# Optimization experiments

Hardware: AMD Instinct MI355X
Metric: run time of the kernel (lower is better)

The kernel has to match this reference:

```python
import jax, jax.numpy as jnp
import numpy as np

B, N, M, E, C_IN, C_OUT = 4, 10000, 10000, 160000, 128, 128


def setup_inputs() -> dict:
    key = jax.random.key(0)
    k1, k2, k3, k4 = jax.random.split(key, 4)
    x = jax.random.normal(k1, (B, N, C_IN), dtype=jnp.float32)
    node_idx = jax.random.randint(k2, (B, 1, E), 0, N)
    hyedge_idx = jax.random.randint(k3, (B, 1, E), 0, M)
    H = jnp.concatenate([node_idx, hyedge_idx], axis=1).astype(jnp.int64)  # [B, 2, E]
    theta = jax.random.normal(k4, (C_IN, C_OUT), dtype=jnp.float32) * (1.0 / np.sqrt(C_IN))
    bias = jnp.zeros((C_OUT,), dtype=jnp.float32)
    return {"x": x, "H": H, "theta": theta, "bias": bias}


def _hyconv_single(xg, Hg):
    # xg: [N, D] (already x @ theta); Hg: [2, E]
    node_idx, hyedge_idx = Hg[0], Hg[1]
    ones = jnp.ones((E,), dtype=xg.dtype)
    # node -> hyperedge: mean over nodes incident to each hyperedge
    deg_e = jax.ops.segment_sum(ones, hyedge_idx, num_segments=M)  # [M]
    e_norm = (1.0 / deg_e)[hyedge_idx]  # [E]
    x_edge = jax.ops.segment_sum(xg[node_idx] * e_norm[:, None], hyedge_idx, num_segments=M)  # [M, D]
    # hyperedge -> node: mean over hyperedges incident to each node
    deg_n = jax.ops.segment_sum(ones, node_idx, num_segments=N)  # [N]
    n_norm = (1.0 / deg_n)[node_idx]  # [E]
    x_node = jax.ops.segment_sum(x_edge[hyedge_idx] * n_norm[:, None], node_idx, num_segments=N)  # [N, D]
    return x_node


def reference(x, H, theta, bias):
    xt = jnp.einsum('bnc,cd->bnd', x, theta)  # dense projection
    out = jax.vmap(_hyconv_single)(xt, H)  # [B, N, D]
    return out + bias
```

## Files before the change

kernel.cpp:

```cpp
#include <hip/hip_runtime.h>
#include <hip/hip_bf16.h>


#define BB 4
#define NN 10000
#define MM 10000
#define EE 160000
#define CC 128
#define BM (BB * MM)
#define BN (BB * NN)
#define NCOPY 8
#define CAPX 16

typedef unsigned short u16;
using bf16 = __hip_bfloat16;
using bf162 = __hip_bfloat162;
typedef unsigned u32x4 __attribute__((ext_vector_type(4)));
typedef float f32x4 __attribute__((ext_vector_type(4)));

__global__ __launch_bounds__(256) void build_gemm_k(const int* __restrict__ H,
                                                    int* __restrict__ ctr,
                                                    u16* __restrict__ srcA,
                                                    u16* __restrict__ srcB,
                                                    const float* __restrict__ x,
                                                    const float* __restrict__ theta,
                                                    bf16* __restrict__ xt) {
    __shared__ float sTh[64 * 128];
    __shared__ float sX[32 * 128];
    const int bi = blockIdx.x;
    const int idx = (bi >> 4) * 8 + (bi & 7);

    if ((bi >> 3) & 1) {
        if (idx >= 1250) return;
        const int gidx = idx * 256 + threadIdx.x;
        const int g0 = gidx * 2;
        const int cp = bi & 7;
        const int b = g0 / EE, e = g0 - b * EE;
        const int2 nd2 = *(const int2*)&H[b * 2 * EE + e];
        const int2 he2 = *(const int2*)&H[b * 2 * EE + EE + e];
        {
            const int bktA = b * MM + he2.x;
            const int s = atomicAdd(&ctr[cp * (BM + BN) + bktA], 1);
            if (s < CAPX) srcA[((size_t)cp * BM + bktA) * CAPX + s] = (u16)nd2.x;
            const int bktB = b * NN + nd2.x;
            const int q = atomicAdd(&ctr[cp * (BM + BN) + BM + bktB], 1);
            if (q < CAPX) srcB[((size_t)cp * BN + bktB) * CAPX + q] = (u16)he2.x;
        }
        {
            const int bktA = b * MM + he2.y;
            const int s = atomicAdd(&ctr[cp * (BM + BN) + bktA], 1);
            if (s < CAPX) srcA[((size_t)cp * BM + bktA) * CAPX + s] = (u16)nd2.y;
            const int bktB = b * NN + nd2.y;
            const int q = atomicAdd(&ctr[cp * (BM + BN) + BM + bktB], 1);
            if (q < CAPX) srcB[((size_t)cp * BN + bktB) * CAPX + q] = (u16)he2.y;
        }
        return;
    }

    if (idx >= 1250) return;
    const int tid = threadIdx.x;
    const int row0 = idx * 32;
    {
        const float4* src = (const float4*)&x[row0 * 128];
        float4* dst = (float4*)sX;
#pragma unroll
        for (int i = 0; i < 4; ++i) dst[tid + 256 * i] = src[tid + 256 * i];
    }
    const int cg2 = (tid & 63) * 2;
    const int rg = tid >> 6;
    float ax[8], ay[8];
#pragma unroll
    for (int r = 0; r < 8; ++r) { ax[r] = 0.f; ay[r] = 0.f; }

    for (int half = 0; half < 2; ++half) {
        __syncthreads();
        {
            const float4* src = (const float4*)&theta[half * 64 * 128];
            float4* dst = (float4*)sTh;
#pragma unroll
            for (int i = 0; i < 8; ++i) dst[tid + 256 * i] = src[tid + 256 * i];
        }
        __syncthreads();
#pragma unroll
        for (int k4 = 0; k4 < 16; ++k4) {
            const int kk = 4 * k4;
            const float2 t0 = *(const float2*)&sTh[(kk + 0) * 128 + cg2];
            const float2 t1 = *(const float2*)&sTh[(kk + 1) * 128 + cg2];
            const float2 t2 = *(const float2*)&sTh[(kk + 2) * 128 + cg2];
            const float2 t3 = *(const float2*)&sTh[(kk + 3) * 128 + cg2];
#pragma unroll
            for (int r = 0; r < 8; ++r) {
                const float4 xv =
                    *(const float4*)&sX[(rg * 8 + r) * 128 + half * 64 + kk];
                ax[r] = fmaf(xv.x, t0.x, ax[r]); ay[r] = fmaf(xv.x, t0.y, ay[r]);
                ax[r] = fmaf(xv.y, t1.x, ax[r]); ay[r] = fmaf(xv.y, t1.y, ay[r]);
                ax[r] = fmaf(xv.z, t2.x, ax[r]); ay[r] = fmaf(xv.z, t2.y, ay[r]);
                ax[r] = fmaf(xv.w, t3.x, ax[r]); ay[r] = fmaf(xv.w, t3.y, ay[r]);
            }
        }
    }
#pragma unroll
    for (int r = 0; r < 8; ++r) {
        bf162 h;
        h.x = __float2bfloat16(ax[r]);
        h.y = __float2bfloat16(ay[r]);
        *(bf162*)&xt[(size_t)(row0 + rg * 8 + r) * 128 + cg2] = h;
    }
}

__device__ __forceinline__ float blo(unsigned w) { return __uint_as_float(w << 16); }
__device__ __forceinline__ float bhi(unsigned w) { return __uint_as_float(w & 0xffff0000u); }
__device__ __forceinline__ unsigned pk2(float a, float b) {
    bf162 h;
    h.x = __float2bfloat16(a);
    h.y = __float2bfloat16(b);
    return *(unsigned*)&h;
}

__device__ __forceinline__ void acc8(const uint4 pk, float* s) {
    s[0] += blo(pk.x); s[1] += bhi(pk.x);
    s[2] += blo(pk.y); s[3] += bhi(pk.y);
    s[4] += blo(pk.z); s[5] += bhi(pk.z);
    s[6] += blo(pk.w); s[7] += bhi(pk.w);
}

__device__ __forceinline__ void swz_bucket(int blk, int tid, int& b, int& wid_local4) {
    const int xcd = blk & 7;
    b = xcd >> 1;
    const int jj = ((blk >> 3) << 1) | (xcd & 1);
    wid_local4 = jj * 4 + (tid >> 6);
}

__global__ __launch_bounds__(256) void phase1_pull(const bf16* __restrict__ xt,
                                                   const int* __restrict__ ctr,
                                                   const u16* __restrict__ srcA,
                                                   const u16* __restrict__ srcB,
                                                   u16* __restrict__ flatB,
                                                   int* __restrict__ cntB,
                                                   bf16* __restrict__ x_edge) {
    __shared__ __align__(16) u16 bufA[4 * 64];
    __shared__ __align__(16) u16 bufB[4 * 64];
    int b, wl;
    swz_bucket(blockIdx.x, threadIdx.x, b, wl);
    const int widA = b * MM + wl;
    const int widB = b * NN + wl;
    const int lane = threadIdx.x & 63;
    const int w4 = threadIdx.x >> 6;
    u16* wbufA = &bufA[w4 * 64];
    u16* wbufB = &bufB[w4 * 64];

    int cA = 0, cB = 0;
    uint4 a0, a1, b0, b1;
    if (lane < NCOPY) {
        const u16* la = srcA + ((size_t)lane * BM + widA) * CAPX;
        const u16* lb = srcB + ((size_t)lane * BN + widB) * CAPX;
        a0 = *(const uint4*)la; a1 = *(const uint4*)(la + 8);
        b0 = *(const uint4*)lb; b1 = *(const uint4*)(lb + 8);
        cA = ctr[lane * (BM + BN) + widA];       cA = cA > CAPX ? CAPX : cA;
        cB = ctr[lane * (BM + BN) + BM + widB];  cB = cB > CAPX ? CAPX : cB;
    }
    int pA = cA, pB = cB;
#pragma unroll
    for (int d = 1; d < 8; d <<= 1) {
        const int oA = __shfl_up(pA, d, 64);
        const int oB = __shfl_up(pB, d, 64);
        if (lane >= d) { pA += oA; pB += oB; }
    }
    const int baseA = pA - cA, baseB = pB - cB;
    int totA = __shfl(pA, 7, 64); totA = totA > 64 ? 64 : totA;
    int totB = __shfl(pB, 7, 64); totB = totB > 64 ? 64 : totB;
    if (lane < NCOPY) {
        const unsigned wa[8] = {a0.x, a0.y, a0.z, a0.w, a1.x, a1.y, a1.z, a1.w};
        const unsigned wb[8] = {b0.x, b0.y, b0.z, b0.w, b1.x, b1.y, b1.z, b1.w};
#pragma unroll
        for (int j = 0; j < CAPX; ++j) {
            const u16 va = (u16)((j & 1) ? (wa[j >> 1] >> 16) : (wa[j >> 1] & 0xffffu));
            const u16 vb = (u16)((j & 1) ? (wb[j >> 1] >> 16) : (wb[j >> 1] & 0xffffu));
            const int pa = baseA + j, pb = baseB + j;
            if (j < cA && pa < 64) wbufA[pa] = va;
            if (j < cB && pb < 64) wbufB[pb] = vb;
        }
    }
    __syncthreads();

    if (lane < 8)
        *(u32x4*)&flatB[(size_t)widB * 64 + lane * 8] = *(const u32x4*)&wbufB[lane * 8];
    if (lane == 0) cntB[widB] = totB;

    const bf16* base = xt + (size_t)b * NN * CC;
    const int g = lane >> 4;
    const int c16 = lane & 15;
    float s[8];
#pragma unroll
    for (int k = 0; k < 8; ++k) s[k] = 0.f;
    int i = 0;
    for (; i + 4 <= totA; i += 4) {
        const int idx = wbufA[i + g];
        const uint4 pk = *(const uint4*)(base + (size_t)idx * CC + c16 * 8);
        acc8(pk, s);
    }
    if (i < totA && g < totA - i) {
        const int idx = wbufA[i + g];
        const uint4 pk = *(const uint4*)(base + (size_t)idx * CC + c16 * 8);
        acc8(pk, s);
    }
#pragma unroll
    for (int k = 0; k < 8; ++k) {
        s[k] += __shfl_xor(s[k], 16, 64);
        s[k] += __shfl_xor(s[k], 32, 64);
    }
    const float w = totA ? 1.0f / (float)totA : 0.f;
    if (g == 0) {
        u32x4 o;
        o.x = pk2(s[0] * w, s[1] * w);
        o.y = pk2(s[2] * w, s[3] * w);
        o.z = pk2(s[4] * w, s[5] * w);
        o.w = pk2(s[6] * w, s[7] * w);
        __builtin_nontemporal_store(o, (u32x4*)&x_edge[(size_t)widA * CC + c16 * 8]);
    }
}

__global__ __launch_bounds__(256) void phase2_pull(const bf16* __restrict__ x_edge,
                                                   const u16* __restrict__ flatB,
                                                   const int* __restrict__ cntB,
                                                   const float* __restrict__ bias,
                                                   float* __restrict__ out) {
    __shared__ __align__(16) u16 buf[4 * 64];
    int b, wl;
    swz_bucket(blockIdx.x, threadIdx.x, b, wl);
    const int wid = b * NN + wl;
    const int lane = threadIdx.x & 63;
    u16* wbuf = &buf[(threadIdx.x >> 6) * 64];
    const int t0 = cntB[wid];
    if (lane < 8)
        *(u32x4*)&wbuf[lane * 8] = *(const u32x4*)&flatB[(size_t)wid * 64 + lane * 8];
    __syncthreads();
    const int total = t0 > 64 ? 64 : t0;

    const bf16* base = x_edge + (size_t)b * MM * CC;
    const int g = lane >> 4;
    const int c16 = lane & 15;
    float s[8];
#pragma unroll
    for (int k = 0; k < 8; ++k) s[k] = 0.f;
    int i = 0;
    for (; i + 4 <= total; i += 4) {
        const int idx = wbuf[i + g];
        const uint4 pk = *(const uint4*)(base + (size_t)idx * CC + c16 * 8);
        acc8(pk, s);
    }
    if (i < total && g < total - i) {
        const int idx = wbuf[i + g];
        const uint4 pk = *(const uint4*)(base + (size_t)idx * CC + c16 * 8);
        acc8(pk, s);
    }
#pragma unroll
    for (int k = 0; k < 8; ++k) {
        s[k] += __shfl_xor(s[k], 16, 64);
        s[k] += __shfl_xor(s[k], 32, 64);
    }
    const float w = total ? 1.0f / (float)total : 0.f;
    if (g < 2) {
        const float4 bv = *(const float4*)&bias[c16 * 8 + g * 4];
        f32x4 o;
        if (g == 0) {
            o.x = s[0] * w + bv.x; o.y = s[1] * w + bv.y;
            o.z = s[2] * w + bv.z; o.w = s[3] * w + bv.w;
        } else {
            o.x = s[4] * w + bv.x; o.y = s[5] * w + bv.y;
            o.z = s[6] * w + bv.z; o.w = s[7] * w + bv.w;
        }
        __builtin_nontemporal_store(o, (f32x4*)&out[(size_t)wid * CC + c16 * 8 + g * 4]);
    }
}

extern "C" void kernel_launch(void* const* d_in, const int* in_sizes, int n_in,
                              void* d_out, int out_size, void* d_ws, size_t ws_size,
                              hipStream_t stream) {
    const float* x = (const float*)d_in[0];
    const int* H = (const int*)d_in[1];
    const float* theta = (const float*)d_in[2];
    const float* bias = (const float*)d_in[3];
    float* out = (float*)d_out;

    bf16* xt = (bf16*)d_ws;
    bf16* x_edge = xt + (size_t)BB * NN * CC;
    int* ctr = (int*)(x_edge + (size_t)BB * MM * CC);
    u16* srcA = (u16*)(ctr + NCOPY * (BM + BN));
    u16* srcB = srcA + (size_t)NCOPY * BM * CAPX;
    u16* flatB = srcB + (size_t)NCOPY * BN * CAPX;
    int* cntB = (int*)(flatB + (size_t)BN * 64);

    hipMemsetAsync(ctr, 0, (size_t)NCOPY * (BM + BN) * sizeof(int), stream);

    build_gemm_k<<<2512, 256, 0, stream>>>(H, ctr, srcA, srcB, x, theta, xt);
    phase1_pull<<<BM / 4, 256, 0, stream>>>(xt, ctr, srcA, srcB, flatB, cntB, x_edge);
    phase2_pull<<<BN / 4, 256, 0, stream>>>(x_edge, flatB, cntB, bias, out);
}
```

Baseline: 179.7 us.

## Remap build/GEMM blocks to XCDs by batch and widen edge-build to four edges per thread

Reworks block-to-work mapping in the fused build/GEMM kernel so each XCD handles GEMM row tiles of a single batch (per-batch tiles with a 16-row tail), and edge-building threads process four edges each via int4 loads, shrinking the grid. The aim is L2 locality of xt per XCD for the later gather phases and fewer atomic-issuing threads. It also switches phase1's x_edge store from nontemporal to a normal store so the data stays cached for phase2. Adds tail-handling branches and changes the atomic ordering pattern.

```diff
diff --git a/kernel.cpp b/kernel.cpp
--- a/kernel.cpp
+++ b/kernel.cpp
@@ -28,43 +28,51 @@
     __shared__ float sTh[64 * 128];
     __shared__ float sX[32 * 128];
     const int bi = blockIdx.x;
-    const int idx = (bi >> 4) * 8 + (bi & 7);
-
-    if ((bi >> 3) & 1) {
-        if (idx >= 1250) return;
-        const int gidx = idx * 256 + threadIdx.x;
-        const int g0 = gidx * 2;
-        const int cp = bi & 7;
+    const int xcd = bi & 7;
+    const int slot = bi >> 3;
+    bool is_gemm;
+    int k;
+    if (slot < 158) { is_gemm = ((slot & 1) == 0); k = slot >> 1; }
+    else            { is_gemm = true;              k = 79 + (slot - 158); }
+
+    if (!is_gemm) {
+        const int w = k * 8 + xcd;
+        if (w >= 625) return;
+        const int g0 = (w * 256 + (int)threadIdx.x) * 4;
+        const int cp = xcd;
         const int b = g0 / EE, e = g0 - b * EE;
-        const int2 nd2 = *(const int2*)&H[b * 2 * EE + e];
-        const int2 he2 = *(const int2*)&H[b * 2 * EE + EE + e];
-        {
-            const int bktA = b * MM + he2.x;
+        const int4 nd4 = *(const int4*)&H[b * 2 * EE + e];
+        const int4 he4 = *(const int4*)&H[b * 2 * EE + EE + e];
+        const int nd[4] = {nd4.x, nd4.y, nd4.z, nd4.w};
+        const int he[4] = {he4.x, he4.y, he4.z, he4.w};
+#pragma unroll
+        for (int t = 0; t < 4; ++t) {
+            const int bktA = b * MM + he[t];
             const int s = atomicAdd(&ctr[cp * (BM + BN) + bktA], 1);
-            if (s < CAPX) srcA[((size_t)cp * BM + bktA) * CAPX + s] = (u16)nd2.x;
-            const int bktB = b * NN + nd2.x;
+            if (s < CAPX) srcA[((size_t)cp * BM + bktA) * CAPX + s] = (u16)nd[t];
+        }
+#pragma unroll
+        for (int t = 0; t < 4; ++t) {
+            const int bktB = b * NN + nd[t];
             const int q = atomicAdd(&ctr[cp * (BM + BN) + BM + bktB], 1);
-            if (q < CAPX) srcB[((size_t)cp * BN + bktB) * CAPX + q] = (u16)he2.x;
-        }
-        {
-            const int bktA = b * MM + he2.y;
-            const int s = atomicAdd(&ctr[cp * (BM + BN) + bktA], 1);
-            if (s < CAPX) srcA[((size_t)cp * BM + bktA) * CAPX + s] = (u16)nd2.y;
-            const int bktB = b * NN + nd2.y;
-            const int q = atomicAdd(&ctr[cp * (BM + BN) + BM + bktB], 1);
-            if (q < CAPX) srcB[((size_t)cp * BN + bktB) * CAPX + q] = (u16)he2.y;
+            if (q < CAPX) srcB[((size_t)cp * BN + bktB) * CAPX + q] = (u16)he[t];
         }
         return;
     }
 
-    if (idx >= 1250) return;
+    const int c = 2 * k + (xcd & 1);
+    if (c >= 313) return;
+    const int b = xcd >> 1;
+    const int row0 = b * NN + c * 32;
+    const int nr = (c == 312) ? 16 : 32;
     const int tid = threadIdx.x;
-    const int row0 = idx * 32;
     {
-        const float4* src = (const float4*)&x[row0 * 128];
+        const float4* src = (const float4*)&x[(size_t)row0 * 128];
         float4* dst = (float4*)sX;
-#pragma unroll
-        for (int i = 0; i < 4; ++i) dst[tid + 256 * i] = src[tid + 256 * i];
+        const int lim = nr * 32;
+#pragma unroll
+        for (int i = 0; i < 4; ++i)
+            if (tid + 256 * i < lim) dst[tid + 256 * i] = src[tid + 256 * i];
     }
     const int cg2 = (tid & 63) * 2;
     const int rg = tid >> 6;
@@ -101,10 +109,12 @@
     }
 #pragma unroll
     for (int r = 0; r < 8; ++r) {
-        bf162 h;
-        h.x = __float2bfloat16(ax[r]);
-        h.y = __float2bfloat16(ay[r]);
-        *(bf162*)&xt[(size_t)(row0 + rg * 8 + r) * 128 + cg2] = h;
+        if (rg * 8 + r < nr) {
+            bf162 h;
+            h.x = __float2bfloat16(ax[r]);
+            h.y = __float2bfloat16(ay[r]);
+            *(bf162*)&xt[(size_t)(row0 + rg * 8 + r) * 128 + cg2] = h;
+        }
     }
 }
 
@@ -216,7 +226,7 @@
         o.y = pk2(s[2] * w, s[3] * w);
         o.z = pk2(s[4] * w, s[5] * w);
         o.w = pk2(s[6] * w, s[7] * w);
-        __builtin_nontemporal_store(o, (u32x4*)&x_edge[(size_t)widA * CC + c16 * 8]);
+        *(u32x4*)&x_edge[(size_t)widA * CC + c16 * 8] = o;
     }
 }
 
@@ -293,7 +303,7 @@
 
     hipMemsetAsync(ctr, 0, (size_t)NCOPY * (BM + BN) * sizeof(int), stream);
 
-    build_gemm_k<<<2512, 256, 0, stream>>>(H, ctr, srcA, srcB, x, theta, xt);
+    build_gemm_k<<<1888, 256, 0, stream>>>(H, ctr, srcA, srcB, x, theta, xt);
     phase1_pull<<<BM / 4, 256, 0, stream>>>(xt, ctr, srcA, srcB, flatB, cntB, x_edge);
     phase2_pull<<<BN / 4, 256, 0, stream>>>(x_edge, flatB, cntB, bias, out);
 }
```

Result: slower. 189.8 us (+5.7%).

## Process four segments per wavefront in pull kernels to cut block count

Applied to the files above, without the earlier changes.

Each wavefront now handles four hyperedges (phase 1) or four nodes (phase 2) instead of one, so both pull kernels launch about a quarter as many blocks. In phase 1 all 64 lanes load the bucket lists in parallel (8 copies for each of 8 segments) rather than only 8 lanes. Four independent gather accumulators per wave add memory-level parallelism and spread the per-block setup and sync cost over more work. In exchange, register pressure rises and wave work becomes less even, since segment degrees vary. The x_edge store also drops its nontemporal hint.

```diff
diff --git a/kernel.cpp b/kernel.cpp
--- a/kernel.cpp
+++ b/kernel.cpp
@@ -61,7 +61,7 @@
     const int tid = threadIdx.x;
     const int row0 = idx * 32;
     {
-        const float4* src = (const float4*)&x[row0 * 128];
+        const float4* src = (const float4*)&x[(size_t)row0 * 128];
         float4* dst = (float4*)sX;
 #pragma unroll
         for (int i = 0; i < 4; ++i) dst[tid + 256 * i] = src[tid + 256 * i];
@@ -124,11 +124,11 @@
     s[6] += blo(pk.w); s[7] += bhi(pk.w);
 }
 
-__device__ __forceinline__ void swz_bucket(int blk, int tid, int& b, int& wid_local4) {
+__device__ __forceinline__ bool swz_grp(int blk, int& b, int& jj) {
     const int xcd = blk & 7;
     b = xcd >> 1;
-    const int jj = ((blk >> 3) << 1) | (xcd & 1);
-    wid_local4 = jj * 4 + (tid >> 6);
+    jj = ((blk >> 3) << 1) | (xcd & 1);
+    return jj < 625;
 }
 
 __global__ __launch_bounds__(256) void phase1_pull(const bf16* __restrict__ xt,
@@ -138,86 +138,100 @@
                                                    u16* __restrict__ flatB,
                                                    int* __restrict__ cntB,
                                                    bf16* __restrict__ x_edge) {
-    __shared__ __align__(16) u16 bufA[4 * 64];
-    __shared__ __align__(16) u16 bufB[4 * 64];
-    int b, wl;
-    swz_bucket(blockIdx.x, threadIdx.x, b, wl);
-    const int widA = b * MM + wl;
-    const int widB = b * NN + wl;
+    __shared__ __align__(16) u16 slot[4][8 * 64];
+    __shared__ u16 hdr[4][8];
+    int b, jj;
+    if (!swz_grp(blockIdx.x, b, jj)) return;
+    const int w4 = threadIdx.x >> 6;
     const int lane = threadIdx.x & 63;
-    const int w4 = threadIdx.x >> 6;
-    u16* wbufA = &bufA[w4 * 64];
-    u16* wbufB = &bufB[w4 * 64];
-
-    int cA = 0, cB = 0;
-    uint4 a0, a1, b0, b1;
-    if (lane < NCOPY) {
-        const u16* la = srcA + ((size_t)lane * BM + widA) * CAPX;
-        const u16* lb = srcB + ((size_t)lane * BN + widB) * CAPX;
-        a0 = *(const uint4*)la; a1 = *(const uint4*)(la + 8);
-        b0 = *(const uint4*)lb; b1 = *(const uint4*)(lb + 8);
-        cA = ctr[lane * (BM + BN) + widA];       cA = cA > CAPX ? CAPX : cA;
-        cB = ctr[lane * (BM + BN) + BM + widB];  cB = cB > CAPX ? CAPX : cB;
-    }
-    int pA = cA, pB = cB;
+    const int wl0 = jj * 16 + w4 * 4;
+    u16* sb = slot[w4];
+    u16* hd = hdr[w4];
+
+    const int t = lane >> 3, c = lane & 7;
+    const bool isA = t < 4;
+    const int wl = wl0 + (isA ? t : t - 4);
+    const int wid = (isA ? b * MM : b * NN) + wl;
+    const u16* lst = isA ? (srcA + ((size_t)c * BM + wid) * CAPX)
+                         : (srcB + ((size_t)c * BN + wid) * CAPX);
+    const uint4 f0 = *(const uint4*)lst;
+    const uint4 f1 = *(const uint4*)(lst + 8);
+    int cnt = ctr[c * (BM + BN) + (isA ? wid : BM + wid)];
+    cnt = cnt > CAPX ? CAPX : cnt;
+    int pre = cnt;
 #pragma unroll
     for (int d = 1; d < 8; d <<= 1) {
-        const int oA = __shfl_up(pA, d, 64);
-        const int oB = __shfl_up(pB, d, 64);
-        if (lane >= d) { pA += oA; pB += oB; }
-    }
-    const int baseA = pA - cA, baseB = pB - cB;
-    int totA = __shfl(pA, 7, 64); totA = totA > 64 ? 64 : totA;
-    int totB = __shfl(pB, 7, 64); totB = totB > 64 ? 64 : totB;
-    if (lane < NCOPY) {
-        const unsigned wa[8] = {a0.x, a0.y, a0.z, a0.w, a1.x, a1.y, a1.z, a1.w};
-        const unsigned wb[8] = {b0.x, b0.y, b0.z, b0.w, b1.x, b1.y, b1.z, b1.w};
+        const int o = __shfl_up(pre, d, 8);
+        if (c >= d) pre += o;
+    }
+    const int base = pre - cnt;
+    if (c == 7) hd[t] = (u16)(pre > 64 ? 64 : pre);
+    {
+        const unsigned wd[8] = {f0.x, f0.y, f0.z, f0.w, f1.x, f1.y, f1.z, f1.w};
 #pragma unroll
         for (int j = 0; j < CAPX; ++j) {
-            const u16 va = (u16)((j & 1) ? (wa[j >> 1] >> 16) : (wa[j >> 1] & 0xffffu));
-            const u16 vb = (u16)((j & 1) ? (wb[j >> 1] >> 16) : (wb[j >> 1] & 0xffffu));
-            const int pa = baseA + j, pb = baseB + j;
-            if (j < cA && pa < 64) wbufA[pa] = va;
-            if (j < cB && pb < 64) wbufB[pb] = vb;
+            const u16 v = (u16)((j & 1) ? (wd[j >> 1] >> 16) : (wd[j >> 1] & 0xffffu));
+            const int p = base + j;
+            if (j < cnt && p < 64) sb[t * 64 + p] = v;
         }
     }
     __syncthreads();
 
-    if (lane < 8)
-        *(u32x4*)&flatB[(size_t)widB * 64 + lane * 8] = *(const u32x4*)&wbufB[lane * 8];
-    if (lane == 0) cntB[widB] = totB;
-
-    const bf16* base = xt + (size_t)b * NN * CC;
-    const int g = lane >> 4;
-    const int c16 = lane & 15;
-    float s[8];
-#pragma unroll
-    for (int k = 0; k < 8; ++k) s[k] = 0.f;
-    int i = 0;
-    for (; i + 4 <= totA; i += 4) {
-        const int idx = wbufA[i + g];
-        const uint4 pk = *(const uint4*)(base + (size_t)idx * CC + c16 * 8);
-        acc8(pk, s);
-    }
-    if (i < totA && g < totA - i) {
-        const int idx = wbufA[i + g];
-        const uint4 pk = *(const uint4*)(base + (size_t)idx * CC + c16 * 8);
-        acc8(pk, s);
-    }
-#pragma unroll
-    for (int k = 0; k < 8; ++k) {
-        s[k] += __shfl_xor(s[k], 16, 64);
-        s[k] += __shfl_xor(s[k], 32, 64);
-    }
-    const float w = totA ? 1.0f / (float)totA : 0.f;
-    if (g == 0) {
-        u32x4 o;
-        o.x = pk2(s[0] * w, s[1] * w);
-        o.y = pk2(s[2] * w, s[3] * w);
-        o.z = pk2(s[4] * w, s[5] * w);
-        o.w = pk2(s[6] * w, s[7] * w);
-        __builtin_nontemporal_store(o, (u32x4*)&x_edge[(size_t)widA * CC + c16 * 8]);
-    }
+    if (lane < 32) {
+        const int tb = lane >> 3, h = lane & 7;
+        const int widB = b * NN + wl0 + tb;
+        *(u32x4*)&flatB[(size_t)widB * 64 + h * 8] =
+            *(const u32x4*)&sb[(4 + tb) * 64 + h * 8];
+        if (h == 0) cntB[widB] = hd[4 + tb];
+    }
+
+    const bf16* bas = xt + (size_t)b * NN * CC;
+    const int g = lane >> 4, c16 = lane & 15;
+    const int T0 = hd[0], T1 = hd[1], T2 = hd[2], T3 = hd[3];
+    float s0[8], s1[8], s2[8], s3[8];
+#pragma unroll
+    for (int k = 0; k < 8; ++k) { s0[k] = 0.f; s1[k] = 0.f; s2[k] = 0.f; s3[k] = 0.f; }
+#define GATH(SS, TT, TOT)                                                              \
+    {                                                                                  \
+        int i = 0;                                                                     \
+        for (; i + 4 <= (TOT); i += 4) {                                               \
+            const int ix = sb[(TT)*64 + i + g];                                        \
+            const uint4 pk = *(const uint4*)(bas + (size_t)ix * CC + c16 * 8);         \
+            acc8(pk, SS);                                                              \
+        }                                                                              \
+        if (i < (TOT) && g < (TOT)-i) {                                                \
+            const int ix = sb[(TT)*64 + i + g];                                        \
+            const uint4 pk = *(const uint4*)(bas + (size_t)ix * CC + c16 * 8);         \
+            acc8(pk, SS);                                                              \
+        }                                                                              \
+    }
+    GATH(s0, 0, T0)
+    GATH(s1, 1, T1)
+    GATH(s2, 2, T2)
+    GATH(s3, 3, T3)
+#undef GATH
+
+#define REDST(SS, TT, TOT)                                                             \
+    {                                                                                  \
+        _Pragma("unroll") for (int k = 0; k < 8; ++k) {                                \
+            SS[k] += __shfl_xor(SS[k], 16, 64);                                        \
+            SS[k] += __shfl_xor(SS[k], 32, 64);                                        \
+        }                                                                              \
+        const float w = (TOT) ? 1.0f / (float)(TOT) : 0.f;                             \
+        if (g == 0) {                                                                  \
+            u32x4 o;                                                                   \
+            o.x = pk2(SS[0] * w, SS[1] * w);                                           \
+            o.y = pk2(SS[2] * w, SS[3] * w);                                           \
+            o.z = pk2(SS[4] * w, SS[5] * w);                                           \
+            o.w = pk2(SS[6] * w, SS[7] * w);                                           \
+            *(u32x4*)&x_edge[(size_t)(b * MM + wl0 + (TT)) * CC + c16 * 8] = o;        \
+        }                                                                              \
+    }
+    REDST(s0, 0, T0)
+    REDST(s1, 1, T1)
+    REDST(s2, 2, T2)
+    REDST(s3, 3, T3)
+#undef REDST
 }
 
 __global__ __launch_bounds__(256) void phase2_pull(const bf16* __restrict__ x_edge,
@@ -225,53 +239,77 @@
                                                    const int* __restrict__ cntB,
                                                    const float* __restrict__ bias,
                                                    float* __restrict__ out) {
-    __shared__ __align__(16) u16 buf[4 * 64];
-    int b, wl;
-    swz_bucket(blockIdx.x, threadIdx.x, b, wl);
-    const int wid = b * NN + wl;
+    __shared__ __align__(16) u16 slot[4][4 * 64];
+    __shared__ int hdr[4][4];
+    int b, jj;
+    if (!swz_grp(blockIdx.x, b, jj)) return;
+    const int w4 = threadIdx.x >> 6;
     const int lane = threadIdx.x & 63;
-    u16* wbuf = &buf[(threadIdx.x >> 6) * 64];
-    const int t0 = cntB[wid];
-    if (lane < 8)
-        *(u32x4*)&wbuf[lane * 8] = *(const u32x4*)&flatB[(size_t)wid * 64 + lane * 8];
+    const int wl0 = jj * 16 + w4 * 4;
+    u16* sb = slot[w4];
+    int* hd = hdr[w4];
+
+    if (lane < 32) {
+        const int tb = lane >> 3, h = lane & 7;
+        const int wid = b * NN + wl0 + tb;
+        *(u32x4*)&sb[tb * 64 + h * 8] =
+            *(const u32x4*)&flatB[(size_t)wid * 64 + h * 8];
+        if (h == 0) hd[tb] = cntB[wid];
+    }
     __syncthreads();
-    const int total = t0 > 64 ? 64 : t0;
-
-    const bf16* base = x_edge + (size_t)b * MM * CC;
-    const int g = lane >> 4;
-    const int c16 = lane & 15;
-    float s[8];
-#pragma unroll
-    for (int k = 0; k < 8; ++k) s[k] = 0.f;
-    int i = 0;
-    for (; i + 4 <= total; i += 4) {
-        const int idx = wbuf[i + g];
-        const uint4 pk = *(const uint4*)(base + (size_t)idx * CC + c16 * 8);
-        acc8(pk, s);
-    }
-    if (i < total && g < total - i) {
-        const int idx = wbuf[i + g];
-        const uint4 pk = *(const uint4*)(base + (size_t)idx * CC + c16 * 8);
-        acc8(pk, s);
-    }
-#pragma unroll
-    for (int k = 0; k < 8; ++k) {
-        s[k] += __shfl_xor(s[k], 16, 64);
-        s[k] += __shfl_xor(s[k], 32, 64);
-    }
-    const float w = total ? 1.0f / (float)total : 0.f;
-    if (g < 2) {
-        const float4 bv = *(const float4*)&bias[c16 * 8 + g * 4];
-        f32x4 o;
-        if (g == 0) {
-            o.x = s[0] * w + bv.x; o.y = s[1] * w + bv.y;
-            o.z = s[2] * w + bv.z; o.w = s[3] * w + bv.w;
-        } else {
-            o.x = s[4] * w + bv.x; o.y = s[5] * w + bv.y;
-            o.z = s[6] * w + bv.z; o.w = s[7] * w + bv.w;
-        }
-        __builtin_nontemporal_store(o, (f32x4*)&out[(size_t)wid * CC + c16 * 8 + g * 4]);
-    }
+
+    const bf16* bas = x_edge + (size_t)b * MM * CC;
+    const int g = lane >> 4, c16 = lane & 15;
+    const int T0 = hd[0], T1 = hd[1], T2 = hd[2], T3 = hd[3];
+    float s0[8], s1[8], s2[8], s3[8];
+#pragma unroll
+    for (int k = 0; k < 8; ++k) { s0[k] = 0.f; s1[k] = 0.f; s2[k] = 0.f; s3[k] = 0.f; }
+#define GATH(SS, TT, TOT)                                                              \
+    {                                                                                  \
+        int i = 0;                                                                     \
+        for (; i + 4 <= (TOT); i += 4) {                                               \
+            const int ix = sb[(TT)*64 + i + g];                                        \
+            const uint4 pk = *(const uint4*)(bas + (size_t)ix * CC + c16 * 8);         \
+            acc8(pk, SS);                                                              \
+        }                                                                              \
+        if (i < (TOT) && g < (TOT)-i) {                                                \
+            const int ix = sb[(TT)*64 + i + g];                                        \
+            const uint4 pk = *(const uint4*)(bas + (size_t)ix * CC + c16 * 8);         \
+            acc8(pk, SS);                                                              \
+        }                                                                              \
+    }
+    GATH(s0, 0, T0)
+    GATH(s1, 1, T1)
+    GATH(s2, 2, T2)
+    GATH(s3, 3, T3)
+#undef GATH
+
+    const float4 bv = *(const float4*)&bias[c16 * 8 + (g & 1) * 4];
+#define REDST(SS, TT, TOT)                                                             \
+    {                                                                                  \
+        _Pragma("unroll") for (int k = 0; k < 8; ++k) {                                \
+            SS[k] += __shfl_xor(SS[k], 16, 64);                                        \
+            SS[k] += __shfl_xor(SS[k], 32, 64);                                        \
+        }                                                                              \
+        const float w = (TOT) ? 1.0f / (float)(TOT) : 0.f;                             \
+        if (g < 2) {                                                                   \
+            f32x4 o;                                                                   \
+            if (g == 0) {                                                              \
+                o.x = SS[0] * w + bv.x; o.y = SS[1] * w + bv.y;                        \
+                o.z = SS[2] * w + bv.z; o.w = SS[3] * w + bv.w;                        \
+            } else {                                                                   \
+                o.x = SS[4] * w + bv.x; o.y = SS[5] * w + bv.y;                        \
+                o.z = SS[6] * w + bv.z; o.w = SS[7] * w + bv.w;                        \
+            }                                                                          \
+            __builtin_nontemporal_store(                                               \
+                o, (f32x4*)&out[(size_t)(b * NN + wl0 + (TT)) * CC + c16 * 8 + g * 4]);\
+        }                                                                              \
+    }
+    REDST(s0, 0, T0)
+    REDST(s1, 1, T1)
+    REDST(s2, 2, T2)
+    REDST(s3, 3, T3)
+#undef REDST
 }
 
 extern "C" void kernel_launch(void* const* d_in, const int* in_sizes, int n_in,
@@ -294,6 +332,6 @@
     hipMemsetAsync(ctr, 0, (size_t)NCOPY * (BM + BN) * sizeof(int), stream);
 
     build_gemm_k<<<2512, 256, 0, stream>>>(H, ctr, srcA, srcB, x, theta, xt);
-    phase1_pull<<<BM / 4, 256, 0, stream>>>(xt, ctr, srcA, srcB, flatB, cntB, x_edge);
-    phase2_pull<<<BN / 4, 256, 0, stream>>>(x_edge, flatB, cntB, bias, out);
-}
+    phase1_pull<<<2504, 256, 0, stream>>>(xt, ctr, srcA, srcB, flatB, cntB, x_edge);
+    phase2_pull<<<2504, 256, 0, stream>>>(x_edge, flatB, cntB, bias, out);
+}
```

Result: faster. 173.0 us (-3.7%).
